# Optimization experiments

Measured on AMD Instinct MI355X. Metric: run time of the kernel, lower is better.

## Reference

```python
import jax, jax.numpy as jnp
import numpy as np

B, S, D, H = 2, 2048, 1024, 16
DK = D // H


def setup_inputs() -> dict:
    key = jax.random.key(0)
    ks = jax.random.split(key, 13)
    scale = 1.0 / np.sqrt(D)
    return {
        "query": jax.random.normal(ks[0], (B, S, D), jnp.float32),
        "key": jax.random.normal(ks[1], (B, S, D), jnp.float32),
        "value": jax.random.normal(ks[2], (B, S, D), jnp.float32),
        "mask": jax.random.randint(ks[3], (B, S, S), 0, 2, jnp.int32),
        "Wq": jax.random.normal(ks[4], (D, D), jnp.float32) * scale,
        "bq": jnp.zeros((D,), jnp.float32),
        "Wk": jax.random.normal(ks[5], (D, D), jnp.float32) * scale,
        "bk": jnp.zeros((D,), jnp.float32),
        "Wv": jax.random.normal(ks[6], (D, D), jnp.float32) * scale,
        "bv": jnp.zeros((D,), jnp.float32),
        "Wo": jax.random.normal(ks[7], (D, D), jnp.float32) * scale,
        "bo": jnp.zeros((D,), jnp.float32),
    }


def _split_heads(x):
    # [B,S,D] -> [B,H,S,DK]
    b, s, _ = x.shape
    return x.reshape(b, s, H, DK).transpose(0, 2, 1, 3)


def reference(query, key, value, mask, Wq, bq, Wk, bk, Wv, bv, Wo, bo):
    q = _split_heads(query @ Wq + bq)
    k = _split_heads(key @ Wk + bk)
    v = _split_heads(value @ Wv + bv)
    # scaled dot-product scores [B,H,Sq,Sk]
    scores = jnp.einsum("bhqd,bhkd->bhqk", q, k) / jnp.sqrt(jnp.float32(DK))
    scores = jnp.where(mask[:, None, :, :] == 0, jnp.float32(-1e9), scores)
    p_attn = jax.nn.softmax(scores, axis=-1)  # dropout p=0.0 -> identity
    x = jnp.einsum("bhqk,bhkd->bhqd", p_attn, v)
    x = x.transpose(0, 2, 1, 3).reshape(query.shape[0], -1, D)
    return x @ Wo + bo
```

## Files before the change

kernel.cpp:

```cpp
#include <hip/hip_runtime.h>
#include <cstdint>

#define B_ 2
#define S_ 2048
#define D_ 1024
#define H_ 16
#define DK_ 64
#define SCALE_ 0.18033688011112042f

typedef float f32x4 __attribute__((ext_vector_type(4)));
typedef float f32x16 __attribute__((ext_vector_type(16)));
typedef __bf16 bf16x8 __attribute__((ext_vector_type(8)));
typedef unsigned short u16x8 __attribute__((ext_vector_type(8)));
typedef unsigned short u16x4 __attribute__((ext_vector_type(4)));
typedef unsigned int u32x4 __attribute__((ext_vector_type(4)));

__device__ __forceinline__ unsigned short f2bf(float x) {
  unsigned int u = __builtin_bit_cast(unsigned int, x);
  u += 0x7FFFu + ((u >> 16) & 1u);
  return (unsigned short)(u >> 16);
}

__device__ __forceinline__ void gload16(const void* g, void* l) {
  __builtin_amdgcn_global_load_lds((__attribute__((address_space(1))) void*)(void*)g,
                                   (__attribute__((address_space(3))) void*)l, 16, 0, 0);
}

__device__ __forceinline__ float exp2v(float x) {
  float r;
  asm("v_exp_f32 %0, %1" : "=v"(r) : "v"(x));
  return r;
}

__device__ __forceinline__ unsigned int cvtpk(float a, float b) {
  unsigned int r;
  asm("v_cvt_pk_bf16_f32 %0, %1, %2" : "=v"(r) : "v"(a), "v"(b));
  return r;
}

__device__ __forceinline__ unsigned int bit_mask(unsigned int w, int bit) {
#if __has_builtin(__builtin_amdgcn_sbfe)
  return (unsigned int)__builtin_amdgcn_sbfe((int)w, bit, 1);
#else
  return (unsigned int)((int)(w << (31 - bit)) >> 31);
#endif
}

__global__ __launch_bounds__(256) void prep_kernel(
    const float* __restrict__ w0, const float* __restrict__ w1,
    const float* __restrict__ w2, const float* __restrict__ w3,
    unsigned short* o0, unsigned short* o1, unsigned short* o2, unsigned short* o3,
    const int* __restrict__ mask, unsigned int* __restrict__ mb) {
  __shared__ float t[32][33];
  const int bid = blockIdx.x;
  const int tid = threadIdx.x;
  if (bid < 4096) {
    const int z = bid >> 10, rr = bid & 1023;
    const float* W;
    unsigned short* O;
    float sc = 1.f;
    if (z == 0) { W = w0; O = o0; sc = SCALE_; }
    else if (z == 1) { W = w1; O = o1; }
    else if (z == 2) { W = w2; O = o2; }
    else { W = w3; O = o3; }
    const int n0 = (rr & 31) * 32, k0 = (rr >> 5) * 32;
    const int tx = tid & 31, ty = tid >> 5;
    for (int i = ty; i < 32; i += 8) t[i][tx] = W[(size_t)(k0 + i) * D_ + n0 + tx];
    __syncthreads();
    for (int i = ty; i < 32; i += 8) O[(size_t)(n0 + i) * D_ + k0 + tx] = f2bf(t[tx][i] * sc);
  } else {
    const int wid = ((bid - 4096) << 2) + (tid >> 6);
    const int lane = tid & 63;
    size_t base = (size_t)wid << 6;
    unsigned long long bits = __ballot(mask[base + lane] != 0);
    if (lane == 0) *(unsigned long long*)(mb + (base >> 5)) = bits;
  }
}

template <int MODE, int TM, int TN, int NWM, int NWN, bool AF32>
__device__ __forceinline__ void gemm_t(const void* __restrict__ Ap,
                                       const unsigned short* __restrict__ BT,
                                       const float* __restrict__ bias, float bsc,
                                       void* __restrict__ Cp,
                                       unsigned short* __restrict__ AlS,
                                       unsigned short* __restrict__ BlS,
                                       int M, int N, int K) {
  static_assert(NWM * NWN == 4, "4 waves");
  constexpr int WM = TM / NWM;
  constexpr int WN = TN / NWN;
  constexpr int MR = WM / 16, NR = WN / 16;
  constexpr int ASTRIDE = TM * 32;
  constexpr int BSTRIDE = TN * 32;
  const unsigned short* A16 = (const unsigned short*)Ap;
  const float* A32 = (const float*)Ap;
  const int tid = threadIdx.x;
  const int lane = tid & 63;
  const int w = tid >> 6;
  const int wr = w / NWN, wc = w % NWN;
  const int nwg = gridDim.x * gridDim.y;
  const int wg = blockIdx.x + gridDim.x * blockIdx.y;
  const int work = (wg & 7) * (nwg >> 3) + (wg >> 3);
  const int nx = N / TN;
  const int m0 = (work / nx) * TM, n0 = (work % nx) * TN;

  f32x4 acc[MR][NR] = {};
  const int nk = K / 32;
  const int srow = lane >> 2;
  const int sxor = ((lane & 3) ^ ((srow >> 1) & 3)) * 8;
  const int scol_lin = (lane & 3) * 8;

  const int fr = lane & 15;
  const int rsw = ((lane >> 4) ^ ((fr >> 1) & 3)) * 8;

  auto stageB = [&](int kt, int bufi) {
#pragma unroll
    for (int it = 0; it < TN / 64; ++it) {
      int chunk = it * 4 + w;
      gload16(BT + (size_t)(n0 + chunk * 16 + srow) * K + kt * 32 + sxor,
              BlS + bufi * BSTRIDE + chunk * 512);
    }
  };
  auto stageA16 = [&](int kt, int bufi) {
#pragma unroll
    for (int it = 0; it < TM / 64; ++it) {
      int chunk = it * 4 + w;
      gload16(A16 + (size_t)(m0 + chunk * 16 + srow) * K + kt * 32 + sxor,
              AlS + bufi * ASTRIDE + chunk * 512);
    }
  };

  auto loadA32 = [&](int kt, f32x4 (&aR)[TM / 64][2]) {
#pragma unroll
    for (int it = 0; it < TM / 64; ++it) {
      int chunk = it * 4 + w;
      const float* ga = A32 + (size_t)(m0 + chunk * 16 + srow) * K + kt * 32 + scol_lin;
      aR[it][0] = *(const f32x4*)ga;
      aR[it][1] = *(const f32x4*)(ga + 4);
    }
  };
  auto writeA = [&](int bufi, f32x4 (&aR)[TM / 64][2]) {
#pragma unroll
    for (int it = 0; it < TM / 64; ++it) {
      int chunk = it * 4 + w;
      u32x4 pk;
      pk[0] = cvtpk(aR[it][0][0], aR[it][0][1]);
      pk[1] = cvtpk(aR[it][0][2], aR[it][0][3]);
      pk[2] = cvtpk(aR[it][1][0], aR[it][1][1]);
      pk[3] = cvtpk(aR[it][1][2], aR[it][1][3]);
      *(u32x4*)(AlS + bufi * ASTRIDE + chunk * 512 + srow * 32 + sxor) = pk;
    }
  };
  auto compute = [&](int bufi) {
    bf16x8 af[MR], bf[NR];
#pragma unroll
    for (int i = 0; i < MR; ++i)
      af[i] = __builtin_bit_cast(bf16x8,
          *(const u16x8*)(AlS + bufi * ASTRIDE + (wr * WM + i * 16 + fr) * 32 + rsw));
#pragma unroll
    for (int j = 0; j < NR; ++j)
      bf[j] = __builtin_bit_cast(bf16x8,
          *(const u16x8*)(BlS + bufi * BSTRIDE + (wc * WN + j * 16 + fr) * 32 + rsw));
    __builtin_amdgcn_s_setprio(1);
#pragma unroll
    for (int i = 0; i < MR; ++i)
#pragma unroll
      for (int j = 0; j < NR; ++j)
        acc[i][j] = __builtin_amdgcn_mfma_f32_16x16x32_bf16(af[i], bf[j], acc[i][j], 0, 0, 0);
    __builtin_amdgcn_s_setprio(0);
  };

  if (AF32) {
    f32x4 aA[TM / 64][2];
    loadA32(0, aA);
    writeA(0, aA);
    stageB(0, 0);
    if (nk > 1) loadA32(1, aA);
    asm volatile("s_waitcnt vmcnt(2) lgkmcnt(0)" ::: "memory");
    __builtin_amdgcn_s_barrier();
    __builtin_amdgcn_sched_barrier(0);
    for (int kt = 0; kt < nk; ++kt) {
      const int b = kt & 1;
      if (kt + 1 < nk) stageB(kt + 1, b ^ 1);
      compute(b);
      if (kt + 1 < nk) writeA(b ^ 1, aA);
      if (kt + 2 < nk) loadA32(kt + 2, aA);
      if (kt + 1 < nk) {
        if (kt + 2 < nk)
          asm volatile("s_waitcnt vmcnt(2) lgkmcnt(0)" ::: "memory");
        else
          asm volatile("s_waitcnt vmcnt(0) lgkmcnt(0)" ::: "memory");
        __builtin_amdgcn_s_barrier();
        __builtin_amdgcn_sched_barrier(0);
      }
    }
  } else {
    stageA16(0, 0);
    stageB(0, 0);
    for (int kt = 0; kt < nk; ++kt) {
      const int buf = kt & 1;
      __syncthreads();
      if (kt + 1 < nk) {
        stageB(kt + 1, buf ^ 1);
        stageA16(kt + 1, buf ^ 1);
      }
      compute(buf);
    }
  }

  const int rg = (lane >> 4) * 4;
  const int cg = lane & 15;
#pragma unroll
  for (int i = 0; i < MR; ++i)
#pragma unroll
    for (int j = 0; j < NR; ++j) {
      int col = n0 + wc * WN + j * 16 + cg;
      float bv = bias[col] * bsc;
#pragma unroll
      for (int e = 0; e < 4; ++e) {
        int row = m0 + wr * WM + i * 16 + rg + e;
        float v = acc[i][j][e] + bv;
        if (MODE == 1)
          ((float*)Cp)[(size_t)row * N + col] = v;
        else if (MODE == 0)
          ((unsigned short*)Cp)[(size_t)row * N + col] = f2bf(v);
        else
          ((unsigned short*)Cp)[((size_t)(row >> 11) * D_ + col) * S_ + (row & (S_ - 1))] = f2bf(v);
      }
    }
}

__global__ __launch_bounds__(256) void qkv_gemm_kernel(
    const float* __restrict__ query, const float* __restrict__ key,
    const float* __restrict__ value, const unsigned short* __restrict__ wtq,
    const unsigned short* __restrict__ wtk, const unsigned short* __restrict__ wtv,
    const float* __restrict__ bq, const float* __restrict__ bk, const float* __restrict__ bv,
    unsigned short* q, unsigned short* k, unsigned short* vt) {
  __shared__ alignas(16) unsigned short As[2 * 64 * 32];
  __shared__ alignas(16) unsigned short Bs[2 * 128 * 32];
  if (blockIdx.z == 0)
    gemm_t<0, 64, 128, 2, 2, true>(query, wtq, bq, SCALE_, (void*)q, As, Bs, B_ * S_, D_, D_);
  else if (blockIdx.z == 1)
    gemm_t<0, 64, 128, 2, 2, true>(key, wtk, bk, 1.f, (void*)k, As, Bs, B_ * S_, D_, D_);
  else
    gemm_t<2, 64, 128, 2, 2, true>(value, wtv, bv, 1.f, (void*)vt, As, Bs, B_ * S_, D_, D_);
}

__global__ __launch_bounds__(256) void out_gemm_kernel(const unsigned short* __restrict__ x,
                                                       const unsigned short* __restrict__ wto,
                                                       const float* __restrict__ bo,
                                                       float* __restrict__ out) {
  __shared__ alignas(16) unsigned short As[2 * 128 * 32];
  __shared__ alignas(16) unsigned short Bs[2 * 64 * 32];
  gemm_t<1, 128, 64, 4, 1, false>(x, wto, bo, 1.f, (void*)out, As, Bs, B_ * S_, D_, D_);
}

__global__ __launch_bounds__(256, 2) void attn_kernel(const unsigned short* __restrict__ Q,
                                                      const unsigned short* __restrict__ K,
                                                      const unsigned short* __restrict__ Vt,
                                                      const unsigned int* __restrict__ mb,
                                                      unsigned short* __restrict__ X) {
  __shared__ unsigned short Kl[2][128 * 64];
  __shared__ unsigned short Vl[2][2][64 * 64];

  const int tid = threadIdx.x;
  const int lane = tid & 63;
  const int w = tid >> 6;
  const int ql = lane & 31;
  const int hi = lane >> 5;

  const int wg = blockIdx.x + gridDim.x * blockIdx.y;
  const int swz = (wg & 7) * 64 + (wg >> 3);
  const int qt = swz & 15;
  const int bh = swz >> 4;
  const int b = bh >> 4, h = bh & 15;
  const int q_g = qt * 128 + w * 32 + ql;

  const size_t qkbase = ((size_t)b * S_) * D_ + h * DK_;
  const size_t vtbase = ((size_t)b * D_ + h * DK_) * S_;

  bf16x8 qf[4];
  {
    const unsigned short* qp = Q + qkbase + (size_t)q_g * D_ + hi * 8;
#pragma unroll
    for (int c = 0; c < 4; ++c)
      qf[c] = __builtin_bit_cast(bf16x8, *(const u16x8*)(qp + c * 16));
  }

  const int lr = lane >> 3;
  const int seg = (lane & 7) ^ lr;
  const unsigned short* Ks = K + qkbase + (size_t)(w * 32 + lr) * D_ + seg * 8;
  const unsigned short* Vs = Vt + vtbase + (size_t)(w * 16 + lr) * S_ + seg * 8;

  auto stage = [&](int kt, int bufi) {
#pragma unroll
    for (int c = 0; c < 4; ++c)
      gload16(Ks + ((size_t)kt * 128 + c * 8) * D_, &Kl[bufi][(w * 32 + c * 8) * 64]);
#pragma unroll
    for (int c = 0; c < 4; ++c)
      gload16(Vs + (size_t)((c & 1) * 8) * S_ + kt * 128 + (c >> 1) * 64,
              &Vl[bufi][c >> 1][(w * 16 + (c & 1) * 8) * 64]);
  };

  const unsigned long long* mrow =
      (const unsigned long long*)mb + ((size_t)b * S_ + q_g) * 32;

  f32x16 o0 = {}, o1 = {};
  f32x16 o2 = {};
  const int sw = (ql & 7) << 4;

  const unsigned int one2 = 0x3F803F80u;
  const bf16x8 onesf = __builtin_bit_cast(bf16x8, u32x4{one2, one2, one2, one2});

  stage(0, 0);
  const int NT = S_ / 128;
  unsigned long long M0n = mrow[0], M1n = mrow[1];

  for (int kt = 0; kt < NT; ++kt) {
    const int buf = kt & 1;
    __syncthreads();
    unsigned long long M0 = M0n, M1 = M1n;

    bf16x8 kf[2][2][4];
#pragma unroll
    for (int hh = 0; hh < 2; ++hh) {
      const char* Kb = (const char*)&Kl[buf][hh * 64 * 64];
#pragma unroll
      for (int r = 0; r < 2; ++r)
#pragma unroll
        for (int c = 0; c < 4; ++c)
          kf[hh][r][c] = __builtin_bit_cast(
              bf16x8, *(const u16x8*)(Kb + (((r * 32 + ql) * 128 + c * 32 + hi * 16) ^ sw)));
    }
    if (kt < NT - 1) {
      stage(kt + 1, buf ^ 1);
      M0n = mrow[kt * 2 + 2];
      M1n = mrow[kt * 2 + 3];
    }

    f32x16 s[2][2] = {};
    __builtin_amdgcn_s_setprio(1);
#pragma unroll
    for (int hh = 0; hh < 2; ++hh)
#pragma unroll
      for (int c = 0; c < 4; ++c) {
        s[hh][0] = __builtin_amdgcn_mfma_f32_32x32x16_bf16(kf[hh][0][c], qf[c], s[hh][0], 0, 0, 0);
        s[hh][1] = __builtin_amdgcn_mfma_f32_32x32x16_bf16(kf[hh][1][c], qf[c], s[hh][1], 0, 0, 0);
      }
    __builtin_amdgcn_s_setprio(0);

    bf16x8 vf[2][2][4];
#pragma unroll
    for (int hh = 0; hh < 2; ++hh) {
      const char* Vb = (const char*)&Vl[buf][hh][0];
#pragma unroll
      for (int nt = 0; nt < 2; ++nt)
#pragma unroll
        for (int kc = 0; kc < 4; ++kc)
          vf[hh][nt][kc] = __builtin_bit_cast(
              bf16x8, *(const u16x8*)(Vb + (((nt * 32 + ql) * 128 + kc * 32 + hi * 16) ^ sw)));
    }

    u32x4 pw[2][4];
#pragma unroll
    for (int hh = 0; hh < 2; ++hh) {
      const unsigned long long M = hh ? M1 : M0;
      unsigned int W0 = (unsigned int)(M >> (hi * 4));
      unsigned int W1 = (unsigned int)(M >> (32 + hi * 4));
#pragma unroll
      for (int r = 0; r < 16; ++r) {
        const int krl = (r & 3) + 8 * (r >> 2);
        unsigned int mk0 = bit_mask(W0, krl);
        float p0 = exp2v(s[hh][0][r]);
        s[hh][0][r] = __builtin_bit_cast(float, __builtin_bit_cast(unsigned int, p0) & mk0);
        unsigned int mk1 = bit_mask(W1, krl);
        float p1 = exp2v(s[hh][1][r]);
        s[hh][1][r] = __builtin_bit_cast(float, __builtin_bit_cast(unsigned int, p1) & mk1);
      }
#pragma unroll
      for (int kc = 0; kc < 4; ++kc) {
        const int rb = (kc & 1) * 8;
        const int st = kc >> 1;
        unsigned int w0 = cvtpk(s[hh][st][rb + 0], s[hh][st][rb + 1]);
        unsigned int w1 = cvtpk(s[hh][st][rb + 2], s[hh][st][rb + 3]);
        unsigned int w2 = cvtpk(s[hh][st][rb + 4], s[hh][st][rb + 5]);
        unsigned int w3 = cvtpk(s[hh][st][rb + 6], s[hh][st][rb + 7]);
        unsigned int u0, u1, u2, u3;
#if __has_builtin(__builtin_amdgcn_permlane32_swap)
        { auto r02 = __builtin_amdgcn_permlane32_swap(w0, w2, false, false);
          u0 = r02[0]; u2 = r02[1]; }
        { auto r13 = __builtin_amdgcn_permlane32_swap(w1, w3, false, false);
          u1 = r13[0]; u3 = r13[1]; }
#else
        { unsigned int t0 = (unsigned int)__shfl_xor((int)w0, 32);
          unsigned int t2 = (unsigned int)__shfl_xor((int)w2, 32);
          u0 = hi ? t2 : w0; u2 = hi ? w2 : t0;
          unsigned int t1 = (unsigned int)__shfl_xor((int)w1, 32);
          unsigned int t3 = (unsigned int)__shfl_xor((int)w3, 32);
          u1 = hi ? t3 : w1; u3 = hi ? w3 : t1; }
#endif
        pw[hh][kc] = u32x4{u0, u1, u2, u3};
      }
    }

    __builtin_amdgcn_s_setprio(1);
#pragma unroll
    for (int hh = 0; hh < 2; ++hh)
#pragma unroll
      for (int kc = 0; kc < 4; ++kc) {
        bf16x8 pf = __builtin_bit_cast(bf16x8, pw[hh][kc]);
        o0 = __builtin_amdgcn_mfma_f32_32x32x16_bf16(vf[hh][0][kc], pf, o0, 0, 0, 0);
        o1 = __builtin_amdgcn_mfma_f32_32x32x16_bf16(vf[hh][1][kc], pf, o1, 0, 0, 0);
        o2 = __builtin_amdgcn_mfma_f32_32x32x16_bf16(onesf, pf, o2, 0, 0, 0);
      }
    __builtin_amdgcn_s_setprio(0);
  }

  float inv = 1.f / o2[0];
  unsigned short* Xp = X + ((size_t)b * S_ + q_g) * D_ + h * DK_;
#pragma unroll
  for (int rb = 0; rb < 4; ++rb) {
    int d0 = 8 * rb + 4 * hi;
    *(unsigned int*)(Xp + d0) = cvtpk(o0[4 * rb + 0] * inv, o0[4 * rb + 1] * inv);
    *(unsigned int*)(Xp + d0 + 2) = cvtpk(o0[4 * rb + 2] * inv, o0[4 * rb + 3] * inv);
    *(unsigned int*)(Xp + 32 + d0) = cvtpk(o1[4 * rb + 0] * inv, o1[4 * rb + 1] * inv);
    *(unsigned int*)(Xp + 32 + d0 + 2) = cvtpk(o1[4 * rb + 2] * inv, o1[4 * rb + 3] * inv);
  }
}

extern "C" void kernel_launch(void* const* d_in, const int* in_sizes, int n_in,
                              void* d_out, int out_size, void* d_ws, size_t ws_size,
                              hipStream_t stream) {
  const float* query = (const float*)d_in[0];
  const float* key = (const float*)d_in[1];
  const float* value = (const float*)d_in[2];
  const int* mask = (const int*)d_in[3];
  const float* Wq = (const float*)d_in[4];
  const float* bq = (const float*)d_in[5];
  const float* Wk = (const float*)d_in[6];
  const float* bk = (const float*)d_in[7];
  const float* Wv = (const float*)d_in[8];
  const float* bv = (const float*)d_in[9];
  const float* Wo = (const float*)d_in[10];
  const float* bo = (const float*)d_in[11];
  float* out = (float*)d_out;

  const size_t ACT = (size_t)B_ * S_ * D_;
  const size_t WSZ = (size_t)D_ * D_;
  unsigned short* ws = (unsigned short*)d_ws;
  unsigned short* wtq = ws;
  unsigned short* wtk = wtq + WSZ;
  unsigned short* wtv = wtk + WSZ;
  unsigned short* wto = wtv + WSZ;
  unsigned short* qb = wto + WSZ;
  unsigned short* kb = qb + ACT;
  unsigned short* vt = kb + ACT;
  unsigned int* mbp = (unsigned int*)(vt + ACT);
  unsigned short* xb = (unsigned short*)(mbp + (size_t)B_ * S_ * S_ / 32);

  prep_kernel<<<36864, 256, 0, stream>>>(Wq, Wk, Wv, Wo, wtq, wtk, wtv, wto, mask, mbp);

  dim3 gg(8, 64, 3);
  qkv_gemm_kernel<<<gg, 256, 0, stream>>>(query, key, value, wtq, wtk, wtv,
                                          bq, bk, bv, qb, kb, vt);

  dim3 ag(S_ / 128, B_ * H_);
  attn_kernel<<<ag, 256, 0, stream>>>(qb, kb, vt, mbp, xb);

  dim3 og(16, 32, 1);
  out_gemm_kernel<<<og, 256, 0, stream>>>(xb, wto, bo, out);
}
```

Measured before the change: 145.3 us.

## Split attention over two key halves and merge partial outputs

The attention kernel now uses a third grid dimension to split the 2048-key range into two halves of 1024 keys, processed in 64-key tiles with smaller shared buffers. Each half writes unnormalized bf16 partial outputs plus per-row softmax denominators to workspace, and a new merge kernel sums the two halves and normalizes. The aim is more blocks in flight and better latency hiding in attention. In exchange it adds an extra kernel launch, extra global traffic for partials, more barriers per key, and precision loss from rounding unnormalized partial sums to bf16. The launch-bounds occupancy hint was also dropped.

Result: slower. 158.3 us (+9.0%).

```diff
diff --git a/kernel.cpp b/kernel.cpp
--- a/kernel.cpp
+++ b/kernel.cpp
@@ -19,6 +19,10 @@
   unsigned int u = __builtin_bit_cast(unsigned int, x);
   u += 0x7FFFu + ((u >> 16) & 1u);
   return (unsigned short)(u >> 16);
+}
+
+__device__ __forceinline__ float bf2f(unsigned short x) {
+  return __builtin_bit_cast(float, (unsigned int)x << 16);
 }
 
 __device__ __forceinline__ void gload16(const void* g, void* l) {
@@ -254,19 +258,21 @@
   gemm_t<1, 128, 64, 4, 1, false>(x, wto, bo, 1.f, (void*)out, As, Bs, B_ * S_, D_, D_);
 }
 
-__global__ __launch_bounds__(256, 2) void attn_kernel(const unsigned short* __restrict__ Q,
-                                                      const unsigned short* __restrict__ K,
-                                                      const unsigned short* __restrict__ Vt,
-                                                      const unsigned int* __restrict__ mb,
-                                                      unsigned short* __restrict__ X) {
-  __shared__ unsigned short Kl[2][128 * 64];
-  __shared__ unsigned short Vl[2][2][64 * 64];
+__global__ __launch_bounds__(256) void attn_kernel(const unsigned short* __restrict__ Q,
+                                                   const unsigned short* __restrict__ K,
+                                                   const unsigned short* __restrict__ Vt,
+                                                   const unsigned int* __restrict__ mb,
+                                                   unsigned short* __restrict__ Op,
+                                                   float* __restrict__ Lp) {
+  __shared__ unsigned short Kl[2][64 * 64];
+  __shared__ unsigned short Vl[2][64 * 64];
 
   const int tid = threadIdx.x;
   const int lane = tid & 63;
   const int w = tid >> 6;
   const int ql = lane & 31;
   const int hi = lane >> 5;
+  const int z = blockIdx.z;
 
   const int wg = blockIdx.x + gridDim.x * blockIdx.y;
   const int swz = (wg & 7) * 64 + (wg >> 3);
@@ -288,21 +294,21 @@
 
   const int lr = lane >> 3;
   const int seg = (lane & 7) ^ lr;
-  const unsigned short* Ks = K + qkbase + (size_t)(w * 32 + lr) * D_ + seg * 8;
-  const unsigned short* Vs = Vt + vtbase + (size_t)(w * 16 + lr) * S_ + seg * 8;
+  const unsigned short* Ks =
+      K + qkbase + ((size_t)z * 1024 + w * 16 + lr) * D_ + seg * 8;
+  const unsigned short* Vs =
+      Vt + vtbase + (size_t)(w * 16 + lr) * S_ + z * 1024 + seg * 8;
 
   auto stage = [&](int kt, int bufi) {
 #pragma unroll
-    for (int c = 0; c < 4; ++c)
-      gload16(Ks + ((size_t)kt * 128 + c * 8) * D_, &Kl[bufi][(w * 32 + c * 8) * 64]);
-#pragma unroll
-    for (int c = 0; c < 4; ++c)
-      gload16(Vs + (size_t)((c & 1) * 8) * S_ + kt * 128 + (c >> 1) * 64,
-              &Vl[bufi][c >> 1][(w * 16 + (c & 1) * 8) * 64]);
+    for (int c = 0; c < 2; ++c) {
+      gload16(Ks + ((size_t)kt * 64 + c * 8) * D_, &Kl[bufi][(w * 16 + c * 8) * 64]);
+      gload16(Vs + (size_t)(c * 8) * S_ + kt * 64, &Vl[bufi][(w * 16 + c * 8) * 64]);
+    }
   };
 
   const unsigned long long* mrow =
-      (const unsigned long long*)mb + ((size_t)b * S_ + q_g) * 32;
+      (const unsigned long long*)mb + ((size_t)b * S_ + q_g) * 32 + z * 16;
 
   f32x16 o0 = {}, o1 = {};
   f32x16 o2 = {};
@@ -312,119 +318,129 @@
   const bf16x8 onesf = __builtin_bit_cast(bf16x8, u32x4{one2, one2, one2, one2});
 
   stage(0, 0);
-  const int NT = S_ / 128;
-  unsigned long long M0n = mrow[0], M1n = mrow[1];
+  const int NT = 1024 / 64;
 
   for (int kt = 0; kt < NT; ++kt) {
     const int buf = kt & 1;
     __syncthreads();
-    unsigned long long M0 = M0n, M1 = M1n;
-
-    bf16x8 kf[2][2][4];
-#pragma unroll
-    for (int hh = 0; hh < 2; ++hh) {
-      const char* Kb = (const char*)&Kl[buf][hh * 64 * 64];
-#pragma unroll
-      for (int r = 0; r < 2; ++r)
-#pragma unroll
-        for (int c = 0; c < 4; ++c)
-          kf[hh][r][c] = __builtin_bit_cast(
-              bf16x8, *(const u16x8*)(Kb + (((r * 32 + ql) * 128 + c * 32 + hi * 16) ^ sw)));
-    }
-    if (kt < NT - 1) {
-      stage(kt + 1, buf ^ 1);
-      M0n = mrow[kt * 2 + 2];
-      M1n = mrow[kt * 2 + 3];
-    }
-
-    f32x16 s[2][2] = {};
+    unsigned long long M = mrow[kt];
+
+    bf16x8 kf[2][4];
+    const char* Kb = (const char*)&Kl[buf][0];
+#pragma unroll
+    for (int r = 0; r < 2; ++r)
+#pragma unroll
+      for (int c = 0; c < 4; ++c)
+        kf[r][c] = __builtin_bit_cast(
+            bf16x8, *(const u16x8*)(Kb + (((r * 32 + ql) * 128 + c * 32 + hi * 16) ^ sw)));
+    if (kt < NT - 1) stage(kt + 1, buf ^ 1);
+
+    f32x16 s0 = {}, s1 = {};
     __builtin_amdgcn_s_setprio(1);
 #pragma unroll
-    for (int hh = 0; hh < 2; ++hh)
-#pragma unroll
-      for (int c = 0; c < 4; ++c) {
-        s[hh][0] = __builtin_amdgcn_mfma_f32_32x32x16_bf16(kf[hh][0][c], qf[c], s[hh][0], 0, 0, 0);
-        s[hh][1] = __builtin_amdgcn_mfma_f32_32x32x16_bf16(kf[hh][1][c], qf[c], s[hh][1], 0, 0, 0);
+    for (int c = 0; c < 4; ++c) {
+      s0 = __builtin_amdgcn_mfma_f32_32x32x16_bf16(kf[0][c], qf[c], s0, 0, 0, 0);
+      s1 = __builtin_amdgcn_mfma_f32_32x32x16_bf16(kf[1][c], qf[c], s1, 0, 0, 0);
+    }
+    __builtin_amdgcn_s_setprio(0);
+
+    bf16x8 vf[2][4];
+    const char* Vb = (const char*)&Vl[buf][0];
+#pragma unroll
+    for (int nt = 0; nt < 2; ++nt)
+#pragma unroll
+      for (int kc = 0; kc < 4; ++kc)
+        vf[nt][kc] = __builtin_bit_cast(
+            bf16x8, *(const u16x8*)(Vb + (((nt * 32 + ql) * 128 + kc * 32 + hi * 16) ^ sw)));
+
+    unsigned int W0 = (unsigned int)(M >> (hi * 4));
+    unsigned int W1 = (unsigned int)(M >> (32 + hi * 4));
+#pragma unroll
+    for (int r = 0; r < 16; ++r) {
+      const int krl = (r & 3) + 8 * (r >> 2);
+      unsigned int mk0 = bit_mask(W0, krl);
+      float p0 = exp2v(s0[r]);
+      s0[r] = __builtin_bit_cast(float, __builtin_bit_cast(unsigned int, p0) & mk0);
+      unsigned int mk1 = bit_mask(W1, krl);
+      float p1 = exp2v(s1[r]);
+      s1[r] = __builtin_bit_cast(float, __builtin_bit_cast(unsigned int, p1) & mk1);
+    }
+    u32x4 pw[4];
+#pragma unroll
+    for (int kc = 0; kc < 4; ++kc) {
+      const int rb = (kc & 1) * 8;
+      float pa0, pa1, pa2, pa3, pa4, pa5, pa6, pa7;
+      if (kc < 2) {
+        pa0 = s0[rb + 0]; pa1 = s0[rb + 1]; pa2 = s0[rb + 2]; pa3 = s0[rb + 3];
+        pa4 = s0[rb + 4]; pa5 = s0[rb + 5]; pa6 = s0[rb + 6]; pa7 = s0[rb + 7];
+      } else {
+        pa0 = s1[rb + 0]; pa1 = s1[rb + 1]; pa2 = s1[rb + 2]; pa3 = s1[rb + 3];
+        pa4 = s1[rb + 4]; pa5 = s1[rb + 5]; pa6 = s1[rb + 6]; pa7 = s1[rb + 7];
       }
+      unsigned int w0 = cvtpk(pa0, pa1), w1 = cvtpk(pa2, pa3);
+      unsigned int w2 = cvtpk(pa4, pa5), w3 = cvtpk(pa6, pa7);
+      unsigned int u0, u1, u2, u3;
+#if __has_builtin(__builtin_amdgcn_permlane32_swap)
+      { auto r02 = __builtin_amdgcn_permlane32_swap(w0, w2, false, false);
+        u0 = r02[0]; u2 = r02[1]; }
+      { auto r13 = __builtin_amdgcn_permlane32_swap(w1, w3, false, false);
+        u1 = r13[0]; u3 = r13[1]; }
+#else
+      { unsigned int t0 = (unsigned int)__shfl_xor((int)w0, 32);
+        unsigned int t2 = (unsigned int)__shfl_xor((int)w2, 32);
+        u0 = hi ? t2 : w0; u2 = hi ? w2 : t0;
+        unsigned int t1 = (unsigned int)__shfl_xor((int)w1, 32);
+        unsigned int t3 = (unsigned int)__shfl_xor((int)w3, 32);
+        u1 = hi ? t3 : w1; u3 = hi ? w3 : t1; }
+#endif
+      pw[kc] = u32x4{u0, u1, u2, u3};
+    }
+
+    __builtin_amdgcn_s_setprio(1);
+#pragma unroll
+    for (int kc = 0; kc < 4; ++kc) {
+      bf16x8 pf = __builtin_bit_cast(bf16x8, pw[kc]);
+      o0 = __builtin_amdgcn_mfma_f32_32x32x16_bf16(vf[0][kc], pf, o0, 0, 0, 0);
+      o1 = __builtin_amdgcn_mfma_f32_32x32x16_bf16(vf[1][kc], pf, o1, 0, 0, 0);
+      o2 = __builtin_amdgcn_mfma_f32_32x32x16_bf16(onesf, pf, o2, 0, 0, 0);
+    }
     __builtin_amdgcn_s_setprio(0);
-
-    bf16x8 vf[2][2][4];
-#pragma unroll
-    for (int hh = 0; hh < 2; ++hh) {
-      const char* Vb = (const char*)&Vl[buf][hh][0];
-#pragma unroll
-      for (int nt = 0; nt < 2; ++nt)
-#pragma unroll
-        for (int kc = 0; kc < 4; ++kc)
-          vf[hh][nt][kc] = __builtin_bit_cast(
-              bf16x8, *(const u16x8*)(Vb + (((nt * 32 + ql) * 128 + kc * 32 + hi * 16) ^ sw)));
-    }
-
-    u32x4 pw[2][4];
-#pragma unroll
-    for (int hh = 0; hh < 2; ++hh) {
-      const unsigned long long M = hh ? M1 : M0;
-      unsigned int W0 = (unsigned int)(M >> (hi * 4));
-      unsigned int W1 = (unsigned int)(M >> (32 + hi * 4));
-#pragma unroll
-      for (int r = 0; r < 16; ++r) {
-        const int krl = (r & 3) + 8 * (r >> 2);
-        unsigned int mk0 = bit_mask(W0, krl);
-        float p0 = exp2v(s[hh][0][r]);
-        s[hh][0][r] = __builtin_bit_cast(float, __builtin_bit_cast(unsigned int, p0) & mk0);
-        unsigned int mk1 = bit_mask(W1, krl);
-        float p1 = exp2v(s[hh][1][r]);
-        s[hh][1][r] = __builtin_bit_cast(float, __builtin_bit_cast(unsigned int, p1) & mk1);
-      }
-#pragma unroll
-      for (int kc = 0; kc < 4; ++kc) {
-        const int rb = (kc & 1) * 8;
-        const int st = kc >> 1;
-        unsigned int w0 = cvtpk(s[hh][st][rb + 0], s[hh][st][rb + 1]);
-        unsigned int w1 = cvtpk(s[hh][st][rb + 2], s[hh][st][rb + 3]);
-        unsigned int w2 = cvtpk(s[hh][st][rb + 4], s[hh][st][rb + 5]);
-        unsigned int w3 = cvtpk(s[hh][st][rb + 6], s[hh][st][rb + 7]);
-        unsigned int u0, u1, u2, u3;
-#if __has_builtin(__builtin_amdgcn_permlane32_swap)
-        { auto r02 = __builtin_amdgcn_permlane32_swap(w0, w2, false, false);
-          u0 = r02[0]; u2 = r02[1]; }
-        { auto r13 = __builtin_amdgcn_permlane32_swap(w1, w3, false, false);
-          u1 = r13[0]; u3 = r13[1]; }
-#else
-        { unsigned int t0 = (unsigned int)__shfl_xor((int)w0, 32);
-          unsigned int t2 = (unsigned int)__shfl_xor((int)w2, 32);
-          u0 = hi ? t2 : w0; u2 = hi ? w2 : t0;
-          unsigned int t1 = (unsigned int)__shfl_xor((int)w1, 32);
-          unsigned int t3 = (unsigned int)__shfl_xor((int)w3, 32);
-          u1 = hi ? t3 : w1; u3 = hi ? w3 : t1; }
-#endif
-        pw[hh][kc] = u32x4{u0, u1, u2, u3};
-      }
-    }
-
-    __builtin_amdgcn_s_setprio(1);
-#pragma unroll
-    for (int hh = 0; hh < 2; ++hh)
-#pragma unroll
-      for (int kc = 0; kc < 4; ++kc) {
-        bf16x8 pf = __builtin_bit_cast(bf16x8, pw[hh][kc]);
-        o0 = __builtin_amdgcn_mfma_f32_32x32x16_bf16(vf[hh][0][kc], pf, o0, 0, 0, 0);
-        o1 = __builtin_amdgcn_mfma_f32_32x32x16_bf16(vf[hh][1][kc], pf, o1, 0, 0, 0);
-        o2 = __builtin_amdgcn_mfma_f32_32x32x16_bf16(onesf, pf, o2, 0, 0, 0);
-      }
-    __builtin_amdgcn_s_setprio(0);
-  }
-
-  float inv = 1.f / o2[0];
-  unsigned short* Xp = X + ((size_t)b * S_ + q_g) * D_ + h * DK_;
+  }
+
+  unsigned short* Xp = Op + (size_t)z * (B_ * S_ * D_) + ((size_t)b * S_ + q_g) * D_ + h * DK_;
 #pragma unroll
   for (int rb = 0; rb < 4; ++rb) {
     int d0 = 8 * rb + 4 * hi;
-    *(unsigned int*)(Xp + d0) = cvtpk(o0[4 * rb + 0] * inv, o0[4 * rb + 1] * inv);
-    *(unsigned int*)(Xp + d0 + 2) = cvtpk(o0[4 * rb + 2] * inv, o0[4 * rb + 3] * inv);
-    *(unsigned int*)(Xp + 32 + d0) = cvtpk(o1[4 * rb + 0] * inv, o1[4 * rb + 1] * inv);
-    *(unsigned int*)(Xp + 32 + d0 + 2) = cvtpk(o1[4 * rb + 2] * inv, o1[4 * rb + 3] * inv);
-  }
+    *(unsigned int*)(Xp + d0) = cvtpk(o0[4 * rb + 0], o0[4 * rb + 1]);
+    *(unsigned int*)(Xp + d0 + 2) = cvtpk(o0[4 * rb + 2], o0[4 * rb + 3]);
+    *(unsigned int*)(Xp + 32 + d0) = cvtpk(o1[4 * rb + 0], o1[4 * rb + 1]);
+    *(unsigned int*)(Xp + 32 + d0 + 2) = cvtpk(o1[4 * rb + 2], o1[4 * rb + 3]);
+  }
+  if (hi == 0 && h == 0)
+    ;
+  if (hi == 0) Lp[((size_t)z * B_ * S_ + (size_t)b * S_ + q_g) * H_ + h] = o2[0];
+}
+
+__global__ __launch_bounds__(256) void merge_kernel(const unsigned short* __restrict__ O0,
+                                                    const unsigned short* __restrict__ O1,
+                                                    const float* __restrict__ L0,
+                                                    const float* __restrict__ L1,
+                                                    unsigned short* __restrict__ xb) {
+  const size_t idx = (size_t)blockIdx.x * 256 + threadIdx.x;
+  const size_t base = idx * 8;
+  const size_t row = base >> 10;
+  const int h = (int)((base >> 6) & (H_ - 1));
+  const float inv = 1.f / (L0[row * H_ + h] + L1[row * H_ + h]);
+  u16x8 a = *(const u16x8*)(O0 + base);
+  u16x8 bb = *(const u16x8*)(O1 + base);
+  u32x4 o;
+#pragma unroll
+  for (int j = 0; j < 4; ++j) {
+    float v0 = (bf2f(a[2 * j]) + bf2f(bb[2 * j])) * inv;
+    float v1 = (bf2f(a[2 * j + 1]) + bf2f(bb[2 * j + 1])) * inv;
+    o[j] = cvtpk(v0, v1);
+  }
+  *(u32x4*)(xb + base) = o;
 }
 
 extern "C" void kernel_launch(void* const* d_in, const int* in_sizes, int n_in,
@@ -455,7 +471,10 @@
   unsigned short* kb = qb + ACT;
   unsigned short* vt = kb + ACT;
   unsigned int* mbp = (unsigned int*)(vt + ACT);
-  unsigned short* xb = (unsigned short*)(mbp + (size_t)B_ * S_ * S_ / 32);
+  unsigned short* O0 = (unsigned short*)(mbp + (size_t)B_ * S_ * S_ / 32);
+  unsigned short* O1 = O0 + ACT;
+  float* Lp = (float*)(O1 + ACT);
+  unsigned short* xb = O0;
 
   prep_kernel<<<36864, 256, 0, stream>>>(Wq, Wk, Wv, Wo, wtq, wtk, wtv, wto, mask, mbp);
 
@@ -463,8 +482,11 @@
   qkv_gemm_kernel<<<gg, 256, 0, stream>>>(query, key, value, wtq, wtk, wtv,
                                           bq, bk, bv, qb, kb, vt);
 
-  dim3 ag(S_ / 128, B_ * H_);
-  attn_kernel<<<ag, 256, 0, stream>>>(qb, kb, vt, mbp, xb);
+  dim3 ag(S_ / 128, B_ * H_, 2);
+  attn_kernel<<<ag, 256, 0, stream>>>(qb, kb, vt, mbp, O0, Lp);
+
+  merge_kernel<<<(B_ * S_ * D_) / (256 * 8), 256, 0, stream>>>(
+      O0, O1, Lp, Lp + (size_t)B_ * S_ * H_, xb);
 
   dim3 og(16, 32, 1);
   out_gemm_kernel<<<og, 256, 0, stream>>>(xb, wto, bo, out);
```
